# Optimization experiments

Measured on AMD Instinct MI355X. Metric: run time of the kernel, lower is better.

Reference implementation:

```python
import jax, jax.numpy as jnp
import numpy as np

EMB = 128
SQRT_EMB = 128 ** 0.5
LOGIT_CLIP = 10.0


def setup_inputs() -> dict:
    key = jax.random.key(0)
    ks = jax.random.split(key, 10)
    B, N, M, D = 128, 512, 512, EMB
    s = 1.0 / np.sqrt(D)
    return {
        "encoded_last_node": jax.random.normal(ks[0], (B, N, D), jnp.float32),
        "load": jax.random.uniform(ks[1], (B, N), jnp.float32),
        "cur_dist": jax.random.uniform(ks[2], (B, N, M), jnp.float32),
        "log_scale": jnp.ones((), jnp.float32),
        "ninf_mask": jnp.zeros((B, N, M), jnp.float32),
        "encoded_nodes": jax.random.normal(ks[3], (B, M, D), jnp.float32),
        "Wq_last": jax.random.normal(ks[4], (D, D + 1), jnp.float32) * s,
        "Wk": jax.random.normal(ks[5], (D, D), jnp.float32) * s,
        "Wv": jax.random.normal(ks[6], (D, D), jnp.float32) * s,
        "alpha1": jnp.ones((1,), jnp.float32),
        "alpha2": jnp.ones((1,), jnp.float32),
    }


def reference(encoded_last_node, load, cur_dist, log_scale, ninf_mask,
              encoded_nodes, Wq_last, Wk, Wv, alpha1, alpha2):
    # set_kv
    k = jnp.einsum('bmd,ed->bme', encoded_nodes, Wk)   # (B,M,D)
    v = jnp.einsum('bmd,ed->bme', encoded_nodes, Wv)   # (B,M,D)
    # query from last node + load
    input_cat = jnp.concatenate([encoded_last_node, load[:, :, None]], axis=2)  # (B,N,D+1)
    q = jnp.einsum('bnc,ec->bne', input_cat, Wq_last)  # (B,N,D)
    # AAFM: exp-bias linear attention with sigmoid gate
    adaptation_bias = -alpha1[0] * log_scale * cur_dist + ninf_mask  # (B,N,M)
    eb = jnp.exp(adaptation_bias)
    ek = jnp.exp(k)
    num = jnp.einsum('bnm,bmd->bnd', eb, ek * v)
    den = jnp.einsum('bnm,bmd->bnd', eb, ek)
    weighted = jnp.nan_to_num(num / den)  # mirrors torch nan_to_num correction
    aafm_out = jax.nn.sigmoid(q) * weighted  # (B,N,D)
    # single-head decode score against encoder embeddings
    score = jnp.einsum('bnd,bmd->bnm', aafm_out, encoded_nodes)
    score_scaled = score / SQRT_EMB - alpha2[0] * log_scale * cur_dist
    score_masked = LOGIT_CLIP * jnp.tanh(score_scaled) + ninf_mask
    probs = jax.nn.softmax(score_masked, axis=-1)
    return probs
```

## Files before the change

kernel.cpp:

```cpp
#include <hip/hip_runtime.h>
#include <math.h>

#define B 128
#define N 512
#define M 512
#define D 128

typedef __attribute__((ext_vector_type(8))) short s16x8;
typedef __attribute__((ext_vector_type(4))) short s16x4;
typedef __attribute__((ext_vector_type(4))) float f32x4;

#define MFMA16(a, b, c) __builtin_amdgcn_mfma_f32_16x16x32_bf16(a, b, c, 0, 0, 0)

__device__ __forceinline__ void gload16(const void* g, void* l) {
    __builtin_amdgcn_global_load_lds(
        (const __attribute__((address_space(1))) unsigned int*)g,
        (__attribute__((address_space(3))) unsigned int*)l, 16, 0, 0);
}

__device__ __forceinline__ float fast_tanh(float x) {
    x = fminf(fmaxf(x, -15.f), 15.f);
    float E = __expf(2.f * x);
    return 1.f - 2.f / (E + 1.f);
}

__device__ __forceinline__ void fsplit(float x, short& h, short& l) {
    unsigned u = __float_as_uint(x);
    h = (short)(u >> 16);
    float fh = __uint_as_float(u & 0xffff0000u);
    l = (short)(__float_as_uint(x - fh) >> 16);
}

__device__ __forceinline__ void fsplit8(float4 x0, float4 x1, s16x8& h, s16x8& l) {
    short a, b;
    fsplit(x0.x, a, b); h[0] = a; l[0] = b;
    fsplit(x0.y, a, b); h[1] = a; l[1] = b;
    fsplit(x0.z, a, b); h[2] = a; l[2] = b;
    fsplit(x0.w, a, b); h[3] = a; l[3] = b;
    fsplit(x1.x, a, b); h[4] = a; l[4] = b;
    fsplit(x1.y, a, b); h[5] = a; l[5] = b;
    fsplit(x1.z, a, b); h[6] = a; l[6] = b;
    fsplit(x1.w, a, b); h[7] = a; l[7] = b;
}

__global__ void k_prep_w(const float* __restrict__ Wk, const float* __restrict__ Wv,
                         const float* __restrict__ Wq,
                         unsigned short* __restrict__ Wk_hi, unsigned short* __restrict__ Wk_lo,
                         unsigned short* __restrict__ Wv_hi, unsigned short* __restrict__ Wv_lo,
                         unsigned short* __restrict__ Wq_hi, unsigned short* __restrict__ Wq_lo) {
    int i = blockIdx.x * 256 + threadIdx.x;
    short h, l;
    if (i < 16384) {
        fsplit(Wk[i], h, l); Wk_hi[i] = (unsigned short)h; Wk_lo[i] = (unsigned short)l;
    } else if (i < 32768) {
        int j = i - 16384;
        fsplit(Wv[j], h, l); Wv_hi[j] = (unsigned short)h; Wv_lo[j] = (unsigned short)l;
    } else {
        int j = i - 32768; int e = j >> 7, d = j & 127;
        fsplit(Wq[e * 129 + d], h, l); Wq_hi[j] = (unsigned short)h; Wq_lo[j] = (unsigned short)l;
    }
}

__global__ __launch_bounds__(256) void k_kv(const float* __restrict__ enc,
        const unsigned short* __restrict__ Wk_hi, const unsigned short* __restrict__ Wk_lo,
        const unsigned short* __restrict__ Wv_hi, const unsigned short* __restrict__ Wv_lo,
        unsigned short* __restrict__ EKT_hi, unsigned short* __restrict__ EKT_lo,
        unsigned short* __restrict__ EKVT_hi, unsigned short* __restrict__ EKVT_lo) {
    int b = blockIdx.y;
    int wave = threadIdx.x >> 6, lane = threadIdx.x & 63;
    int row = lane & 15, kg = lane >> 4;
    int m0 = blockIdx.x * 64 + wave * 16;
    f32x4 acc[16];
#pragma unroll
    for (int i = 0; i < 16; i++) acc[i] = (f32x4)0.f;
    const float* ap = enc + ((size_t)b * M + m0 + row) * D + kg * 8;
#pragma unroll
    for (int ks = 0; ks < 4; ks++) {
        float4 x0 = *(const float4*)(ap + ks * 32);
        float4 x1 = *(const float4*)(ap + ks * 32 + 4);
        s16x8 ah, al;
        fsplit8(x0, x1, ah, al);
        int wb = ks * 32 + kg * 8;
#pragma unroll
        for (int ct = 0; ct < 8; ct++) {
            int e = ct * 16 + row;
            s16x8 bh = *(const s16x8*)(Wk_hi + e * D + wb);
            s16x8 bl = *(const s16x8*)(Wk_lo + e * D + wb);
            acc[ct] = MFMA16(ah, bh, acc[ct]);
            acc[ct] = MFMA16(al, bh, acc[ct]);
            acc[ct] = MFMA16(ah, bl, acc[ct]);
            bh = *(const s16x8*)(Wv_hi + e * D + wb);
            bl = *(const s16x8*)(Wv_lo + e * D + wb);
            acc[8 + ct] = MFMA16(ah, bh, acc[8 + ct]);
            acc[8 + ct] = MFMA16(al, bh, acc[8 + ct]);
            acc[8 + ct] = MFMA16(ah, bl, acc[8 + ct]);
        }
    }
#pragma unroll
    for (int ct = 0; ct < 8; ct++) {
        int e = ct * 16 + row;
        s16x4 ekh, ekl, evh, evl;
#pragma unroll
        for (int r = 0; r < 4; r++) {
            float ek = __expf(acc[ct][r]);
            float ev = ek * acc[8 + ct][r];
            short h, l;
            fsplit(ek, h, l); ekh[r] = h; ekl[r] = l;
            fsplit(ev, h, l); evh[r] = h; evl[r] = l;
        }
        int m = m0 + kg * 4;
        int chunk = (m & 31) >> 3;
        int p = chunk ^ (e & 3);
        size_t o = ((size_t)b * D + e) * M + (size_t)(m & ~31) + p * 8 + (m & 7);
        *(s16x4*)(EKT_hi + o) = ekh;
        *(s16x4*)(EKT_lo + o) = ekl;
        *(s16x4*)(EKVT_hi + o) = evh;
        *(s16x4*)(EKVT_lo + o) = evl;
    }
}

__global__ __launch_bounds__(256) void k_q(const float* __restrict__ encl,
        const float* __restrict__ loadv, const float* __restrict__ Wq,
        const unsigned short* __restrict__ Wq_hi, const unsigned short* __restrict__ Wq_lo,
        float* __restrict__ SQ) {
    int b = blockIdx.y;
    int wave = threadIdx.x >> 6, lane = threadIdx.x & 63;
    int row = lane & 15, kg = lane >> 4;
    int n0 = blockIdx.x * 64 + wave * 16;
    f32x4 acc[8];
#pragma unroll
    for (int i = 0; i < 8; i++) acc[i] = (f32x4)0.f;
    const float* ap = encl + ((size_t)b * N + n0 + row) * D + kg * 8;
#pragma unroll
    for (int ks = 0; ks < 4; ks++) {
        float4 x0 = *(const float4*)(ap + ks * 32);
        float4 x1 = *(const float4*)(ap + ks * 32 + 4);
        s16x8 ah, al;
        fsplit8(x0, x1, ah, al);
        int wb = ks * 32 + kg * 8;
#pragma unroll
        for (int ct = 0; ct < 8; ct++) {
            int e = ct * 16 + row;
            s16x8 bh = *(const s16x8*)(Wq_hi + e * D + wb);
            s16x8 bl = *(const s16x8*)(Wq_lo + e * D + wb);
            acc[ct] = MFMA16(ah, bh, acc[ct]);
            acc[ct] = MFMA16(al, bh, acc[ct]);
            acc[ct] = MFMA16(ah, bl, acc[ct]);
        }
    }
#pragma unroll
    for (int r = 0; r < 4; r++) {
        int n = n0 + kg * 4 + r;
        float lv = loadv[(size_t)b * N + n];
        size_t ro = ((size_t)b * N + n) * D;
#pragma unroll
        for (int ct = 0; ct < 8; ct++) {
            int e = ct * 16 + row;
            float q = acc[ct][r] + lv * Wq[e * 129 + 128];
            SQ[ro + e] = 1.f / (1.f + __expf(-q));
        }
    }
}

__global__ __launch_bounds__(256) void k_numden(
        const float* __restrict__ cd, const float* __restrict__ ninf,
        const unsigned short* __restrict__ EKVT_hi, const unsigned short* __restrict__ EKVT_lo,
        const unsigned short* __restrict__ EKT_hi, const unsigned short* __restrict__ EKT_lo,
        float* __restrict__ SQ,
        const float* __restrict__ a1p, const float* __restrict__ lsp) {
    int o = blockIdx.x;
    int jj = o >> 3;
    int b = (o & 7) + ((jj >> 3) << 3);
    int nb = jj & 7;
    int w = threadIdx.x >> 6, lane = threadIdx.x & 63;
    int row = lane & 15, kg = lane >> 4;
    int n0 = nb * 64 + w * 16;
    __shared__ __align__(16) char lds[2][32768];
    float a1ls = a1p[0] * lsp[0];
    const char* gbase = (const char*)(w == 0 ? EKVT_hi : w == 1 ? EKVT_lo
                                    : w == 2 ? EKT_hi : EKT_lo)
                        + (size_t)b * D * M * 2;
    int srow = lane >> 2, schunk = lane & 3;
    f32x4 acc[16];
#pragma unroll
    for (int i = 0; i < 16; i++) acc[i] = (f32x4)0.f;
    const float* cdp = cd + ((size_t)b * N + n0 + row) * M + kg * 8;
    const float* nfp = ninf + ((size_t)b * N + n0 + row) * M + kg * 8;
    int rb = row * 64 + ((kg ^ (row & 3)) << 4);

#define STAGE_ND(buf, mt)                                                          \
    _Pragma("unroll")                                                              \
    for (int jv = 0; jv < 8; jv++) {                                               \
        gload16(gbase + (size_t)(jv * 16 + srow) * 1024 + (mt) * 64 + schunk * 16, \
                lds[buf] + w * 8192 + jv * 1024 + lane * 16);                      \
    }

    float4 c0 = *(const float4*)(cdp), c1 = *(const float4*)(cdp + 4);
    float4 f0 = *(const float4*)(nfp), f1 = *(const float4*)(nfp + 4);
    STAGE_ND(0, 0)

#pragma unroll
    for (int mt = 0; mt < 16; mt++) {
        int cur = mt & 1;
        __syncthreads();
        float4 e0, e1;
        e0.x = __expf(fmaf(-a1ls, c0.x, f0.x));
        e0.y = __expf(fmaf(-a1ls, c0.y, f0.y));
        e0.z = __expf(fmaf(-a1ls, c0.z, f0.z));
        e0.w = __expf(fmaf(-a1ls, c0.w, f0.w));
        e1.x = __expf(fmaf(-a1ls, c1.x, f1.x));
        e1.y = __expf(fmaf(-a1ls, c1.y, f1.y));
        e1.z = __expf(fmaf(-a1ls, c1.z, f1.z));
        e1.w = __expf(fmaf(-a1ls, c1.w, f1.w));
        s16x8 ah, al;
        fsplit8(e0, e1, ah, al);
        if (mt < 15) {
            int m = (mt + 1) * 32;
            c0 = *(const float4*)(cdp + m); c1 = *(const float4*)(cdp + m + 4);
            f0 = *(const float4*)(nfp + m); f1 = *(const float4*)(nfp + m + 4);
            STAGE_ND(cur ^ 1, mt + 1)
        }
#pragma unroll
        for (int ct = 0; ct < 8; ct++) {
            int ro = ct * 1024 + rb;
            s16x8 bh = *(const s16x8*)(&lds[cur][ro]);
            s16x8 bl = *(const s16x8*)(&lds[cur][8192 + ro]);
            acc[ct] = MFMA16(ah, bh, acc[ct]);
            acc[ct] = MFMA16(al, bh, acc[ct]);
            acc[ct] = MFMA16(ah, bl, acc[ct]);
            bh = *(const s16x8*)(&lds[cur][16384 + ro]);
            bl = *(const s16x8*)(&lds[cur][24576 + ro]);
            acc[8 + ct] = MFMA16(ah, bh, acc[8 + ct]);
            acc[8 + ct] = MFMA16(al, bh, acc[8 + ct]);
            acc[8 + ct] = MFMA16(ah, bl, acc[8 + ct]);
        }
    }
#pragma unroll
    for (int r = 0; r < 4; r++) {
        int n = n0 + kg * 4 + r;
        size_t ro = ((size_t)b * N + n) * D;
#pragma unroll
        for (int ct = 0; ct < 8; ct++) {
            int e = ct * 16 + row;
            float num = acc[ct][r], den = acc[8 + ct][r];
            float ww = (den != 0.f) ? num / den : 0.f;
            float aafm = SQ[ro + e] * ww;
            unsigned u = __float_as_uint(aafm);
            unsigned hi = u >> 16;
            float fh = __uint_as_float(u & 0xffff0000u);
            unsigned lo = __float_as_uint(aafm - fh) >> 16;
            SQ[ro + e] = __uint_as_float(hi | (lo << 16));
        }
    }
}

__global__ void k_encsplit(const float* __restrict__ enc,
                           unsigned short* __restrict__ Eh, unsigned short* __restrict__ El) {
    size_t i = (size_t)blockIdx.x * 256 + threadIdx.x;
    size_t bm = i >> 4;
    int c = (int)(i & 15);
    int m = (int)(bm & 511);
    int p = c ^ (m & 7);
    const float* src = enc + bm * 128 + c * 8;
    float4 x0 = *(const float4*)(src);
    float4 x1 = *(const float4*)(src + 4);
    s16x8 h, l;
    fsplit8(x0, x1, h, l);
    *(s16x8*)(Eh + bm * 128 + p * 8) = h;
    *(s16x8*)(El + bm * 128 + p * 8) = l;
}

__global__ __launch_bounds__(256) void k_score(
        const float* __restrict__ AAFM,
        const unsigned short* __restrict__ Eh, const unsigned short* __restrict__ El,
        const float* __restrict__ cd, const float* __restrict__ ninf,
        const float* __restrict__ a2p, const float* __restrict__ lsp,
        float* __restrict__ out) {
    int o = blockIdx.x;
    int j = o >> 3;
    int b = (o & 7) + ((j >> 4) << 3);
    int nb = j & 15;
    int n0 = nb * 32;
    int w = threadIdx.x >> 6, lane = threadIdx.x & 63;
    int row = lane & 15, kg = lane >> 4;
    int ng = w >> 1, mh = w & 1;
    __shared__ __align__(16) char lds[2][32768];
    __shared__ float redm[64][2];
    __shared__ float reds[64][2];
    float a2ls = a2p[0] * lsp[0];
    const float invs = 0.08838834764831845f;

    const float* apk = AAFM + ((size_t)b * N + n0 + ng * 16 + row) * D + kg * 8;
    s16x8 ah[4], al[4];
#pragma unroll
    for (int es = 0; es < 4; es++) {
        float4 w0 = *(const float4*)(apk + es * 32);
        float4 w1 = *(const float4*)(apk + es * 32 + 4);
        unsigned u;
        u = __float_as_uint(w0.x); ah[es][0] = (short)(u & 0xffff); al[es][0] = (short)(u >> 16);
        u = __float_as_uint(w0.y); ah[es][1] = (short)(u & 0xffff); al[es][1] = (short)(u >> 16);
        u = __float_as_uint(w0.z); ah[es][2] = (short)(u & 0xffff); al[es][2] = (short)(u >> 16);
        u = __float_as_uint(w0.w); ah[es][3] = (short)(u & 0xffff); al[es][3] = (short)(u >> 16);
        u = __float_as_uint(w1.x); ah[es][4] = (short)(u & 0xffff); al[es][4] = (short)(u >> 16);
        u = __float_as_uint(w1.y); ah[es][5] = (short)(u & 0xffff); al[es][5] = (short)(u >> 16);
        u = __float_as_uint(w1.z); ah[es][6] = (short)(u & 0xffff); al[es][6] = (short)(u >> 16);
        u = __float_as_uint(w1.w); ah[es][7] = (short)(u & 0xffff); al[es][7] = (short)(u >> 16);
    }
    f32x4 acc[16];
#pragma unroll
    for (int i = 0; i < 16; i++) acc[i] = (f32x4)0.f;

#define STAGE_SC(buf, mc)                                                              \
    _Pragma("unroll")                                                                  \
    for (int jv = 0; jv < 8; jv++) {                                                   \
        int flat = w * 8 + jv;                                                         \
        int arr = flat >> 4, wi = flat & 15;                                           \
        const unsigned short* gb = arr ? El : Eh;                                      \
        const char* src = (const char*)gb                                             \
            + ((size_t)b * M + (mc) * 64 + wi * 4 + kg) * 256 + row * 16;              \
        gload16(src, lds[buf] + arr * 16384 + wi * 1024 + lane * 16);                  \
    }

    STAGE_SC(0, 0)
#pragma unroll
    for (int mc = 0; mc < 8; mc++) {
        int cur = mc & 1;
        __syncthreads();
#pragma unroll
        for (int ct = 0; ct < 2; ct++) {
            int mloc = mh * 32 + ct * 16 + row;
            int a = mc * 2 + ct;
            int rbase = mloc * 256;
            int sw = mloc & 7;
#pragma unroll
            for (int es = 0; es < 4; es++) {
                int ph = (4 * es + kg) ^ sw;
                s16x8 bh = *(const s16x8*)(&lds[cur][rbase + ph * 16]);
                s16x8 bl = *(const s16x8*)(&lds[cur][16384 + rbase + ph * 16]);
                acc[a] = MFMA16(ah[es], bh, acc[a]);
                acc[a] = MFMA16(al[es], bh, acc[a]);
                acc[a] = MFMA16(ah[es], bl, acc[a]);
            }
        }
        float cdv[2][4], nfv[2][4];
#pragma unroll
        for (int ct = 0; ct < 2; ct++)
#pragma unroll
            for (int r = 0; r < 4; r++) {
                size_t idx = ((size_t)b * N + n0 + ng * 16 + kg * 4 + r) * M
                           + (size_t)mc * 64 + mh * 32 + ct * 16 + row;
                cdv[ct][r] = cd[idx];
                nfv[ct][r] = ninf[idx];
            }
        if (mc < 7) STAGE_SC(cur ^ 1, mc + 1)
#pragma unroll
        for (int ct = 0; ct < 2; ct++) {
            int a = mc * 2 + ct;
#pragma unroll
            for (int r = 0; r < 4; r++) {
                acc[a][r] = 10.f * fast_tanh(fmaf(acc[a][r], invs, -a2ls * cdv[ct][r]))
                          + nfv[ct][r];
            }
        }
    }
    float mx[4], sm[4];
#pragma unroll
    for (int r = 0; r < 4; r++) {
        float m = acc[0][r];
#pragma unroll
        for (int a = 1; a < 16; a++) m = fmaxf(m, acc[a][r]);
#pragma unroll
        for (int s = 1; s < 16; s <<= 1) m = fmaxf(m, __shfl_xor(m, s, 64));
        mx[r] = m;
    }
    int rl = ng * 16 + kg * 4;
    if (row == 0) {
#pragma unroll
        for (int r = 0; r < 4; r++) redm[rl + r][mh] = mx[r];
    }
    __syncthreads();
#pragma unroll
    for (int r = 0; r < 4; r++) {
        float m = fmaxf(redm[rl + r][0], redm[rl + r][1]);
        float s = 0.f;
#pragma unroll
        for (int a = 0; a < 16; a++) {
            float e = __expf(acc[a][r] - m);
            acc[a][r] = e;
            s += e;
        }
#pragma unroll
        for (int sh = 1; sh < 16; sh <<= 1) s += __shfl_xor(s, sh, 64);
        sm[r] = s;
    }
    if (row == 0) {
#pragma unroll
        for (int r = 0; r < 4; r++) reds[rl + r][mh] = sm[r];
    }
    __syncthreads();
    float inv[4];
#pragma unroll
    for (int r = 0; r < 4; r++)
        inv[r] = 1.f / (reds[rl + r][0] + reds[rl + r][1]);
#pragma unroll
    for (int a = 0; a < 16; a++) {
        int mc = a >> 1, ct = a & 1;
        size_t mb = (size_t)mc * 64 + mh * 32 + ct * 16 + row;
#pragma unroll
        for (int r = 0; r < 4; r++) {
            int n = n0 + ng * 16 + kg * 4 + r;
            out[((size_t)b * N + n) * M + mb] = acc[a][r] * inv[r];
        }
    }
}

extern "C" void kernel_launch(void* const* d_in, const int* in_sizes, int n_in,
                              void* d_out, int out_size, void* d_ws, size_t ws_size,
                              hipStream_t stream) {
    const float* encl  = (const float*)d_in[0];
    const float* loadv = (const float*)d_in[1];
    const float* cdist = (const float*)d_in[2];
    const float* ls    = (const float*)d_in[3];
    const float* ninf  = (const float*)d_in[4];
    const float* enc   = (const float*)d_in[5];
    const float* Wq    = (const float*)d_in[6];
    const float* Wk    = (const float*)d_in[7];
    const float* Wv    = (const float*)d_in[8];
    const float* a1    = (const float*)d_in[9];
    const float* a2    = (const float*)d_in[10];
    char* ws = (char*)d_ws;
    unsigned short* EKT_hi  = (unsigned short*)(ws);
    unsigned short* EKT_lo  = (unsigned short*)(ws + 16777216);
    unsigned short* EKVT_hi = (unsigned short*)(ws + 33554432);
    unsigned short* EKVT_lo = (unsigned short*)(ws + 50331648);
    float*          SQ      = (float*)(ws + 67108864);
    unsigned short* Wk_hi   = (unsigned short*)(ws + 100663296);
    unsigned short* Wk_lo   = (unsigned short*)(ws + 100663296 + 32768);
    unsigned short* Wv_hi   = (unsigned short*)(ws + 100663296 + 65536);
    unsigned short* Wv_lo   = (unsigned short*)(ws + 100663296 + 98304);
    unsigned short* Wq_hi   = (unsigned short*)(ws + 100663296 + 131072);
    unsigned short* Wq_lo   = (unsigned short*)(ws + 100663296 + 163840);
    unsigned short* ENC_hi  = EKT_hi;
    unsigned short* ENC_lo  = EKT_lo;
    float* out = (float*)d_out;

    k_prep_w<<<192, 256, 0, stream>>>(Wk, Wv, Wq, Wk_hi, Wk_lo, Wv_hi, Wv_lo, Wq_hi, Wq_lo);
    k_kv<<<dim3(8, 128), 256, 0, stream>>>(enc, Wk_hi, Wk_lo, Wv_hi, Wv_lo,
                                           EKT_hi, EKT_lo, EKVT_hi, EKVT_lo);
    k_q<<<dim3(8, 128), 256, 0, stream>>>(encl, loadv, Wq, Wq_hi, Wq_lo, SQ);
    k_numden<<<1024, 256, 0, stream>>>(cdist, ninf, EKVT_hi, EKVT_lo,
                                       EKT_hi, EKT_lo, SQ, a1, ls);
    k_encsplit<<<4096, 256, 0, stream>>>(enc, ENC_hi, ENC_lo);
    k_score<<<2048, 256, 0, stream>>>(SQ, ENC_hi, ENC_lo, cdist, ninf, a2, ls, out);
}
```

Measured before the change: 376.7 us.

## Double rows per wave in numden and score kernels to reuse staged B tiles

```diff
diff --git a/kernel.cpp b/kernel.cpp
--- a/kernel.cpp
+++ b/kernel.cpp
@@ -41,6 +41,20 @@
     fsplit(x1.y, a, b); h[5] = a; l[5] = b;
     fsplit(x1.z, a, b); h[6] = a; l[6] = b;
     fsplit(x1.w, a, b); h[7] = a; l[7] = b;
+}
+
+__device__ __forceinline__ void ebsplit(float4 c0, float4 c1, float4 f0, float4 f1,
+                                        float a1ls, s16x8& ah, s16x8& al) {
+    float4 e0, e1;
+    e0.x = __expf(fmaf(-a1ls, c0.x, f0.x));
+    e0.y = __expf(fmaf(-a1ls, c0.y, f0.y));
+    e0.z = __expf(fmaf(-a1ls, c0.z, f0.z));
+    e0.w = __expf(fmaf(-a1ls, c0.w, f0.w));
+    e1.x = __expf(fmaf(-a1ls, c1.x, f1.x));
+    e1.y = __expf(fmaf(-a1ls, c1.y, f1.y));
+    e1.z = __expf(fmaf(-a1ls, c1.z, f1.z));
+    e1.w = __expf(fmaf(-a1ls, c1.w, f1.w));
+    fsplit8(e0, e1, ah, al);
 }
 
 __global__ void k_prep_w(const float* __restrict__ Wk, const float* __restrict__ Wv,
@@ -162,30 +176,34 @@
     }
 }
 
-__global__ __launch_bounds__(256) void k_numden(
+__global__ __launch_bounds__(256, 2) void k_numden(
         const float* __restrict__ cd, const float* __restrict__ ninf,
         const unsigned short* __restrict__ EKVT_hi, const unsigned short* __restrict__ EKVT_lo,
         const unsigned short* __restrict__ EKT_hi, const unsigned short* __restrict__ EKT_lo,
         float* __restrict__ SQ,
         const float* __restrict__ a1p, const float* __restrict__ lsp) {
     int o = blockIdx.x;
-    int jj = o >> 3;
-    int b = (o & 7) + ((jj >> 3) << 3);
-    int nb = jj & 7;
+    int xcd = o & 7, j = o >> 3;
+    int b = ((j >> 2) << 3) + xcd;
+    int nb = j & 3;
     int w = threadIdx.x >> 6, lane = threadIdx.x & 63;
     int row = lane & 15, kg = lane >> 4;
-    int n0 = nb * 64 + w * 16;
+    int n0 = nb * 128 + w * 32;
     __shared__ __align__(16) char lds[2][32768];
     float a1ls = a1p[0] * lsp[0];
     const char* gbase = (const char*)(w == 0 ? EKVT_hi : w == 1 ? EKVT_lo
                                     : w == 2 ? EKT_hi : EKT_lo)
                         + (size_t)b * D * M * 2;
     int srow = lane >> 2, schunk = lane & 3;
-    f32x4 acc[16];
-#pragma unroll
-    for (int i = 0; i < 16; i++) acc[i] = (f32x4)0.f;
-    const float* cdp = cd + ((size_t)b * N + n0 + row) * M + kg * 8;
-    const float* nfp = ninf + ((size_t)b * N + n0 + row) * M + kg * 8;
+    f32x4 accN[2][8], accD[2][8];
+#pragma unroll
+    for (int s = 0; s < 2; s++)
+#pragma unroll
+        for (int i = 0; i < 8; i++) { accN[s][i] = (f32x4)0.f; accD[s][i] = (f32x4)0.f; }
+    const float* cdp0 = cd + ((size_t)b * N + n0 + row) * M + kg * 8;
+    const float* nfp0 = ninf + ((size_t)b * N + n0 + row) * M + kg * 8;
+    const float* cdp1 = cdp0 + (size_t)16 * M;
+    const float* nfp1 = nfp0 + (size_t)16 * M;
     int rb = row * 64 + ((kg ^ (row & 3)) << 4);
 
 #define STAGE_ND(buf, mt)                                                          \
@@ -195,29 +213,25 @@
                 lds[buf] + w * 8192 + jv * 1024 + lane * 16);                      \
     }
 
-    float4 c0 = *(const float4*)(cdp), c1 = *(const float4*)(cdp + 4);
-    float4 f0 = *(const float4*)(nfp), f1 = *(const float4*)(nfp + 4);
+    float4 c00 = *(const float4*)(cdp0), c01 = *(const float4*)(cdp0 + 4);
+    float4 f00 = *(const float4*)(nfp0), f01 = *(const float4*)(nfp0 + 4);
+    float4 c10 = *(const float4*)(cdp1), c11 = *(const float4*)(cdp1 + 4);
+    float4 f10 = *(const float4*)(nfp1), f11 = *(const float4*)(nfp1 + 4);
     STAGE_ND(0, 0)
 
-#pragma unroll
+#pragma unroll 2
     for (int mt = 0; mt < 16; mt++) {
         int cur = mt & 1;
         __syncthreads();
-        float4 e0, e1;
-        e0.x = __expf(fmaf(-a1ls, c0.x, f0.x));
-        e0.y = __expf(fmaf(-a1ls, c0.y, f0.y));
-        e0.z = __expf(fmaf(-a1ls, c0.z, f0.z));
-        e0.w = __expf(fmaf(-a1ls, c0.w, f0.w));
-        e1.x = __expf(fmaf(-a1ls, c1.x, f1.x));
-        e1.y = __expf(fmaf(-a1ls, c1.y, f1.y));
-        e1.z = __expf(fmaf(-a1ls, c1.z, f1.z));
-        e1.w = __expf(fmaf(-a1ls, c1.w, f1.w));
-        s16x8 ah, al;
-        fsplit8(e0, e1, ah, al);
+        s16x8 ah0, al0, ah1, al1;
+        ebsplit(c00, c01, f00, f01, a1ls, ah0, al0);
+        ebsplit(c10, c11, f10, f11, a1ls, ah1, al1);
         if (mt < 15) {
             int m = (mt + 1) * 32;
-            c0 = *(const float4*)(cdp + m); c1 = *(const float4*)(cdp + m + 4);
-            f0 = *(const float4*)(nfp + m); f1 = *(const float4*)(nfp + m + 4);
+            c00 = *(const float4*)(cdp0 + m); c01 = *(const float4*)(cdp0 + m + 4);
+            f00 = *(const float4*)(nfp0 + m); f01 = *(const float4*)(nfp0 + m + 4);
+            c10 = *(const float4*)(cdp1 + m); c11 = *(const float4*)(cdp1 + m + 4);
+            f10 = *(const float4*)(nfp1 + m); f11 = *(const float4*)(nfp1 + m + 4);
             STAGE_ND(cur ^ 1, mt + 1)
         }
 #pragma unroll
@@ -225,31 +239,40 @@
             int ro = ct * 1024 + rb;
             s16x8 bh = *(const s16x8*)(&lds[cur][ro]);
             s16x8 bl = *(const s16x8*)(&lds[cur][8192 + ro]);
-            acc[ct] = MFMA16(ah, bh, acc[ct]);
-            acc[ct] = MFMA16(al, bh, acc[ct]);
-            acc[ct] = MFMA16(ah, bl, acc[ct]);
+            accN[0][ct] = MFMA16(ah0, bh, accN[0][ct]);
+            accN[0][ct] = MFMA16(al0, bh, accN[0][ct]);
+            accN[0][ct] = MFMA16(ah0, bl, accN[0][ct]);
+            accN[1][ct] = MFMA16(ah1, bh, accN[1][ct]);
+            accN[1][ct] = MFMA16(al1, bh, accN[1][ct]);
+            accN[1][ct] = MFMA16(ah1, bl, accN[1][ct]);
             bh = *(const s16x8*)(&lds[cur][16384 + ro]);
             bl = *(const s16x8*)(&lds[cur][24576 + ro]);
-            acc[8 + ct] = MFMA16(ah, bh, acc[8 + ct]);
-            acc[8 + ct] = MFMA16(al, bh, acc[8 + ct]);
-            acc[8 + ct] = MFMA16(ah, bl, acc[8 + ct]);
-        }
-    }
-#pragma unroll
-    for (int r = 0; r < 4; r++) {
-        int n = n0 + kg * 4 + r;
-        size_t ro = ((size_t)b * N + n) * D;
-#pragma unroll
-        for (int ct = 0; ct < 8; ct++) {
-            int e = ct * 16 + row;
-            float num = acc[ct][r], den = acc[8 + ct][r];
-            float ww = (den != 0.f) ? num / den : 0.f;
-            float aafm = SQ[ro + e] * ww;
-            unsigned u = __float_as_uint(aafm);
-            unsigned hi = u >> 16;
-            float fh = __uint_as_float(u & 0xffff0000u);
-            unsigned lo = __float_as_uint(aafm - fh) >> 16;
-            SQ[ro + e] = __uint_as_float(hi | (lo << 16));
+            accD[0][ct] = MFMA16(ah0, bh, accD[0][ct]);
+            accD[0][ct] = MFMA16(al0, bh, accD[0][ct]);
+            accD[0][ct] = MFMA16(ah0, bl, accD[0][ct]);
+            accD[1][ct] = MFMA16(ah1, bh, accD[1][ct]);
+            accD[1][ct] = MFMA16(al1, bh, accD[1][ct]);
+            accD[1][ct] = MFMA16(ah1, bl, accD[1][ct]);
+        }
+    }
+#pragma unroll
+    for (int s = 0; s < 2; s++) {
+#pragma unroll
+        for (int r = 0; r < 4; r++) {
+            int n = n0 + s * 16 + kg * 4 + r;
+            size_t ro = ((size_t)b * N + n) * D;
+#pragma unroll
+            for (int ct = 0; ct < 8; ct++) {
+                int e = ct * 16 + row;
+                float num = accN[s][ct][r], den = accD[s][ct][r];
+                float ww = (den != 0.f) ? num / den : 0.f;
+                float aafm = SQ[ro + e] * ww;
+                unsigned u = __float_as_uint(aafm);
+                unsigned hi = u >> 16;
+                float fh = __uint_as_float(u & 0xffff0000u);
+                unsigned lo = __float_as_uint(aafm - fh) >> 16;
+                SQ[ro + e] = __uint_as_float(hi | (lo << 16));
+            }
         }
     }
 }
@@ -270,17 +293,17 @@
     *(s16x8*)(El + bm * 128 + p * 8) = l;
 }
 
-__global__ __launch_bounds__(256) void k_score(
+__global__ __launch_bounds__(256, 2) void k_score(
         const float* __restrict__ AAFM,
         const unsigned short* __restrict__ Eh, const unsigned short* __restrict__ El,
         const float* __restrict__ cd, const float* __restrict__ ninf,
         const float* __restrict__ a2p, const float* __restrict__ lsp,
         float* __restrict__ out) {
     int o = blockIdx.x;
-    int j = o >> 3;
-    int b = (o & 7) + ((j >> 4) << 3);
-    int nb = j & 15;
-    int n0 = nb * 32;
+    int xcd = o & 7, j = o >> 3;
+    int b = ((j >> 3) << 3) + xcd;
+    int nb = j & 7;
+    int n0 = nb * 64;
     int w = threadIdx.x >> 6, lane = threadIdx.x & 63;
     int row = lane & 15, kg = lane >> 4;
     int ng = w >> 1, mh = w & 1;
@@ -290,25 +313,30 @@
     float a2ls = a2p[0] * lsp[0];
     const float invs = 0.08838834764831845f;
 
-    const float* apk = AAFM + ((size_t)b * N + n0 + ng * 16 + row) * D + kg * 8;
-    s16x8 ah[4], al[4];
-#pragma unroll
-    for (int es = 0; es < 4; es++) {
-        float4 w0 = *(const float4*)(apk + es * 32);
-        float4 w1 = *(const float4*)(apk + es * 32 + 4);
-        unsigned u;
-        u = __float_as_uint(w0.x); ah[es][0] = (short)(u & 0xffff); al[es][0] = (short)(u >> 16);
-        u = __float_as_uint(w0.y); ah[es][1] = (short)(u & 0xffff); al[es][1] = (short)(u >> 16);
-        u = __float_as_uint(w0.z); ah[es][2] = (short)(u & 0xffff); al[es][2] = (short)(u >> 16);
-        u = __float_as_uint(w0.w); ah[es][3] = (short)(u & 0xffff); al[es][3] = (short)(u >> 16);
-        u = __float_as_uint(w1.x); ah[es][4] = (short)(u & 0xffff); al[es][4] = (short)(u >> 16);
-        u = __float_as_uint(w1.y); ah[es][5] = (short)(u & 0xffff); al[es][5] = (short)(u >> 16);
-        u = __float_as_uint(w1.z); ah[es][6] = (short)(u & 0xffff); al[es][6] = (short)(u >> 16);
-        u = __float_as_uint(w1.w); ah[es][7] = (short)(u & 0xffff); al[es][7] = (short)(u >> 16);
-    }
-    f32x4 acc[16];
-#pragma unroll
-    for (int i = 0; i < 16; i++) acc[i] = (f32x4)0.f;
+    s16x8 ah[2][4], al[2][4];
+#pragma unroll
+    for (int s = 0; s < 2; s++) {
+        const float* apk = AAFM + ((size_t)b * N + n0 + ng * 32 + s * 16 + row) * D + kg * 8;
+#pragma unroll
+        for (int es = 0; es < 4; es++) {
+            float4 w0 = *(const float4*)(apk + es * 32);
+            float4 w1 = *(const float4*)(apk + es * 32 + 4);
+            unsigned u;
+            u = __float_as_uint(w0.x); ah[s][es][0] = (short)(u & 0xffff); al[s][es][0] = (short)(u >> 16);
+            u = __float_as_uint(w0.y); ah[s][es][1] = (short)(u & 0xffff); al[s][es][1] = (short)(u >> 16);
+            u = __float_as_uint(w0.z); ah[s][es][2] = (short)(u & 0xffff); al[s][es][2] = (short)(u >> 16);
+            u = __float_as_uint(w0.w); ah[s][es][3] = (short)(u & 0xffff); al[s][es][3] = (short)(u >> 16);
+            u = __float_as_uint(w1.x); ah[s][es][4] = (short)(u & 0xffff); al[s][es][4] = (short)(u >> 16);
+            u = __float_as_uint(w1.y); ah[s][es][5] = (short)(u & 0xffff); al[s][es][5] = (short)(u >> 16);
+            u = __float_as_uint(w1.z); ah[s][es][6] = (short)(u & 0xffff); al[s][es][6] = (short)(u >> 16);
+            u = __float_as_uint(w1.w); ah[s][es][7] = (short)(u & 0xffff); al[s][es][7] = (short)(u >> 16);
+        }
+    }
+    f32x4 acc[2][16];
+#pragma unroll
+    for (int s = 0; s < 2; s++)
+#pragma unroll
+        for (int i = 0; i < 16; i++) acc[s][i] = (f32x4)0.f;
 
 #define STAGE_SC(buf, mc)                                                              \
     _Pragma("unroll")                                                                  \
@@ -337,79 +365,95 @@
                 int ph = (4 * es + kg) ^ sw;
                 s16x8 bh = *(const s16x8*)(&lds[cur][rbase + ph * 16]);
                 s16x8 bl = *(const s16x8*)(&lds[cur][16384 + rbase + ph * 16]);
-                acc[a] = MFMA16(ah[es], bh, acc[a]);
-                acc[a] = MFMA16(al[es], bh, acc[a]);
-                acc[a] = MFMA16(ah[es], bl, acc[a]);
+                acc[0][a] = MFMA16(ah[0][es], bh, acc[0][a]);
+                acc[0][a] = MFMA16(al[0][es], bh, acc[0][a]);
+                acc[0][a] = MFMA16(ah[0][es], bl, acc[0][a]);
+                acc[1][a] = MFMA16(ah[1][es], bh, acc[1][a]);
+                acc[1][a] = MFMA16(al[1][es], bh, acc[1][a]);
+                acc[1][a] = MFMA16(ah[1][es], bl, acc[1][a]);
             }
         }
-        float cdv[2][4], nfv[2][4];
-#pragma unroll
-        for (int ct = 0; ct < 2; ct++)
-#pragma unroll
-            for (int r = 0; r < 4; r++) {
-                size_t idx = ((size_t)b * N + n0 + ng * 16 + kg * 4 + r) * M
-                           + (size_t)mc * 64 + mh * 32 + ct * 16 + row;
-                cdv[ct][r] = cd[idx];
-                nfv[ct][r] = ninf[idx];
+        float cdv[2][2][4], nfv[2][2][4];
+#pragma unroll
+        for (int s = 0; s < 2; s++)
+#pragma unroll
+            for (int ct = 0; ct < 2; ct++)
+#pragma unroll
+                for (int r = 0; r < 4; r++) {
+                    size_t idx = ((size_t)b * N + n0 + ng * 32 + s * 16 + kg * 4 + r) * M
+                               + (size_t)mc * 64 + mh * 32 + ct * 16 + row;
+                    cdv[s][ct][r] = cd[idx];
+                    nfv[s][ct][r] = ninf[idx];
+                }
+        if (mc < 7) STAGE_SC(cur ^ 1, mc + 1)
+#pragma unroll
+        for (int s = 0; s < 2; s++)
+#pragma unroll
+            for (int ct = 0; ct < 2; ct++) {
+                int a = mc * 2 + ct;
+#pragma unroll
+                for (int r = 0; r < 4; r++) {
+                    acc[s][a][r] = 10.f * fast_tanh(fmaf(acc[s][a][r], invs,
+                                                         -a2ls * cdv[s][ct][r]))
+                                 + nfv[s][ct][r];
+                }
             }
-        if (mc < 7) STAGE_SC(cur ^ 1, mc + 1)
-#pragma unroll
-        for (int ct = 0; ct < 2; ct++) {
-            int a = mc * 2 + ct;
-#pragma unroll
-            for (int r = 0; r < 4; r++) {
-                acc[a][r] = 10.f * fast_tanh(fmaf(acc[a][r], invs, -a2ls * cdv[ct][r]))
-                          + nfv[ct][r];
+    }
+    float mx[2][4], sm[2][4];
+#pragma unroll
+    for (int s = 0; s < 2; s++)
+#pragma unroll
+        for (int r = 0; r < 4; r++) {
+            float m = acc[s][0][r];
+#pragma unroll
+            for (int a = 1; a < 16; a++) m = fmaxf(m, acc[s][a][r]);
+#pragma unroll
+            for (int sh = 1; sh < 16; sh <<= 1) m = fmaxf(m, __shfl_xor(m, sh, 64));
+            mx[s][r] = m;
+        }
+    if (row == 0) {
+#pragma unroll
+        for (int s = 0; s < 2; s++)
+#pragma unroll
+            for (int r = 0; r < 4; r++) redm[ng * 32 + s * 16 + kg * 4 + r][mh] = mx[s][r];
+    }
+    __syncthreads();
+#pragma unroll
+    for (int s = 0; s < 2; s++)
+#pragma unroll
+        for (int r = 0; r < 4; r++) {
+            int rl = ng * 32 + s * 16 + kg * 4 + r;
+            float m = fmaxf(redm[rl][0], redm[rl][1]);
+            float sum = 0.f;
+#pragma unroll
+            for (int a = 0; a < 16; a++) {
+                float e = __expf(acc[s][a][r] - m);
+                acc[s][a][r] = e;
+                sum += e;
             }
-        }
-    }
-    float mx[4], sm[4];
-#pragma unroll
-    for (int r = 0; r < 4; r++) {
-        float m = acc[0][r];
-#pragma unroll
-        for (int a = 1; a < 16; a++) m = fmaxf(m, acc[a][r]);
-#pragma unroll
-        for (int s = 1; s < 16; s <<= 1) m = fmaxf(m, __shfl_xor(m, s, 64));
-        mx[r] = m;
-    }
-    int rl = ng * 16 + kg * 4;
+#pragma unroll
+            for (int sh = 1; sh < 16; sh <<= 1) sum += __shfl_xor(sum, sh, 64);
+            sm[s][r] = sum;
+        }
     if (row == 0) {
 #pragma unroll
-        for (int r = 0; r < 4; r++) redm[rl + r][mh] = mx[r];
+        for (int s = 0; s < 2; s++)
+#pragma unroll
+            for (int r = 0; r < 4; r++) reds[ng * 32 + s * 16 + kg * 4 + r][mh] = sm[s][r];
     }
     __syncthreads();
 #pragma unroll
-    for (int r = 0; r < 4; r++) {
-        float m = fmaxf(redm[rl + r][0], redm[rl + r][1]);
-        float s = 0.f;
-#pragma unroll
-        for (int a = 0; a < 16; a++) {
-            float e = __expf(acc[a][r] - m);
-            acc[a][r] = e;
-            s += e;
-        }
-#pragma unroll
-        for (int sh = 1; sh < 16; sh <<= 1) s += __shfl_xor(s, sh, 64);
-        sm[r] = s;
-    }
-    if (row == 0) {
-#pragma unroll
-        for (int r = 0; r < 4; r++) reds[rl + r][mh] = sm[r];
-    }
-    __syncthreads();
-    float inv[4];
-#pragma unroll
-    for (int r = 0; r < 4; r++)
-        inv[r] = 1.f / (reds[rl + r][0] + reds[rl + r][1]);
-#pragma unroll
-    for (int a = 0; a < 16; a++) {
-        int mc = a >> 1, ct = a & 1;
-        size_t mb = (size_t)mc * 64 + mh * 32 + ct * 16 + row;
+    for (int s = 0; s < 2; s++) {
 #pragma unroll
         for (int r = 0; r < 4; r++) {
-            int n = n0 + ng * 16 + kg * 4 + r;
-            out[((size_t)b * N + n) * M + mb] = acc[a][r] * inv[r];
+            int rl = ng * 32 + s * 16 + kg * 4 + r;
+            float inv = 1.f / (reds[rl][0] + reds[rl][1]);
+            size_t ro = ((size_t)b * N + n0 + rl) * M;
+#pragma unroll
+            for (int a = 0; a < 16; a++) {
+                size_t mb = (size_t)(a >> 1) * 64 + mh * 32 + (a & 1) * 16 + row;
+                out[ro + mb] = acc[s][a][r] * inv;
+            }
         }
     }
 }
@@ -448,8 +492,8 @@
     k_kv<<<dim3(8, 128), 256, 0, stream>>>(enc, Wk_hi, Wk_lo, Wv_hi, Wv_lo,
                                            EKT_hi, EKT_lo, EKVT_hi, EKVT_lo);
     k_q<<<dim3(8, 128), 256, 0, stream>>>(encl, loadv, Wq, Wq_hi, Wq_lo, SQ);
-    k_numden<<<1024, 256, 0, stream>>>(cdist, ninf, EKVT_hi, EKVT_lo,
-                                       EKT_hi, EKT_lo, SQ, a1, ls);
+    k_numden<<<512, 256, 0, stream>>>(cdist, ninf, EKVT_hi, EKVT_lo,
+                                      EKT_hi, EKT_lo, SQ, a1, ls);
     k_encsplit<<<4096, 256, 0, stream>>>(enc, ENC_hi, ENC_lo);
-    k_score<<<2048, 256, 0, stream>>>(SQ, ENC_hi, ENC_lo, cdist, ninf, a2, ls, out);
-}
+    k_score<<<1024, 256, 0, stream>>>(SQ, ENC_hi, ENC_lo, cdist, ninf, a2, ls, out);
+}
```

Measured after the change: 363.5 us. 3.5% less time.

## Switch numden to 32x32 MFMA tiles and halve LDS stages for occupancy

Applied to the files above, without the earlier changes.

```diff
diff --git a/kernel.cpp b/kernel.cpp
--- a/kernel.cpp
+++ b/kernel.cpp
@@ -9,8 +9,10 @@
 typedef __attribute__((ext_vector_type(8))) short s16x8;
 typedef __attribute__((ext_vector_type(4))) short s16x4;
 typedef __attribute__((ext_vector_type(4))) float f32x4;
+typedef __attribute__((ext_vector_type(16))) float f32x16;
 
 #define MFMA16(a, b, c) __builtin_amdgcn_mfma_f32_16x16x32_bf16(a, b, c, 0, 0, 0)
+#define MFMA32(a, b, c) __builtin_amdgcn_mfma_f32_32x32x16_bf16(a, b, c, 0, 0, 0)
 
 __device__ __forceinline__ void gload16(const void* g, void* l) {
     __builtin_amdgcn_global_load_lds(
@@ -41,6 +43,20 @@
     fsplit(x1.y, a, b); h[5] = a; l[5] = b;
     fsplit(x1.z, a, b); h[6] = a; l[6] = b;
     fsplit(x1.w, a, b); h[7] = a; l[7] = b;
+}
+
+__device__ __forceinline__ void ebsplit(float4 c0, float4 c1, float4 f0, float4 f1,
+                                        float a1ls, s16x8& ah, s16x8& al) {
+    float4 e0, e1;
+    e0.x = __expf(fmaf(-a1ls, c0.x, f0.x));
+    e0.y = __expf(fmaf(-a1ls, c0.y, f0.y));
+    e0.z = __expf(fmaf(-a1ls, c0.z, f0.z));
+    e0.w = __expf(fmaf(-a1ls, c0.w, f0.w));
+    e1.x = __expf(fmaf(-a1ls, c1.x, f1.x));
+    e1.y = __expf(fmaf(-a1ls, c1.y, f1.y));
+    e1.z = __expf(fmaf(-a1ls, c1.z, f1.z));
+    e1.w = __expf(fmaf(-a1ls, c1.w, f1.w));
+    fsplit8(e0, e1, ah, al);
 }
 
 __global__ void k_prep_w(const float* __restrict__ Wk, const float* __restrict__ Wv,
@@ -108,10 +124,8 @@
             fsplit(ek, h, l); ekh[r] = h; ekl[r] = l;
             fsplit(ev, h, l); evh[r] = h; evl[r] = l;
         }
-        int m = m0 + kg * 4;
-        int chunk = (m & 31) >> 3;
-        int p = chunk ^ (e & 3);
-        size_t o = ((size_t)b * D + e) * M + (size_t)(m & ~31) + p * 8 + (m & 7);
+        int p = (kg >> 1) ^ (e & 1);
+        size_t o = ((size_t)b * D + e) * M + m0 + p * 8 + (kg & 1) * 4;
         *(s16x4*)(EKT_hi + o) = ekh;
         *(s16x4*)(EKT_lo + o) = ekl;
         *(s16x4*)(EKVT_hi + o) = evh;
@@ -162,94 +176,100 @@
     }
 }
 
-__global__ __launch_bounds__(256) void k_numden(
+__global__ __launch_bounds__(256, 3) void k_numden(
         const float* __restrict__ cd, const float* __restrict__ ninf,
         const unsigned short* __restrict__ EKVT_hi, const unsigned short* __restrict__ EKVT_lo,
         const unsigned short* __restrict__ EKT_hi, const unsigned short* __restrict__ EKT_lo,
         float* __restrict__ SQ,
         const float* __restrict__ a1p, const float* __restrict__ lsp) {
     int o = blockIdx.x;
-    int jj = o >> 3;
-    int b = (o & 7) + ((jj >> 3) << 3);
-    int nb = jj & 7;
+    int xcd = o & 7, j = o >> 3;
+    int b = ((j >> 3) << 3) + xcd;
+    int nb = j & 7;
     int w = threadIdx.x >> 6, lane = threadIdx.x & 63;
-    int row = lane & 15, kg = lane >> 4;
-    int n0 = nb * 64 + w * 16;
-    __shared__ __align__(16) char lds[2][32768];
+    int ng = w >> 1, eh = w & 1;
+    int col = lane & 31, kh = lane >> 5;
+    int n0 = nb * 64 + ng * 32;
+    __shared__ __align__(16) char lds[2][16384];
     float a1ls = a1p[0] * lsp[0];
     const char* gbase = (const char*)(w == 0 ? EKVT_hi : w == 1 ? EKVT_lo
                                     : w == 2 ? EKT_hi : EKT_lo)
                         + (size_t)b * D * M * 2;
-    int srow = lane >> 2, schunk = lane & 3;
-    f32x4 acc[16];
-#pragma unroll
-    for (int i = 0; i < 16; i++) acc[i] = (f32x4)0.f;
-    const float* cdp = cd + ((size_t)b * N + n0 + row) * M + kg * 8;
-    const float* nfp = ninf + ((size_t)b * N + n0 + row) * M + kg * 8;
-    int rb = row * 64 + ((kg ^ (row & 3)) << 4);
-
-#define STAGE_ND(buf, mt)                                                          \
-    _Pragma("unroll")                                                              \
-    for (int jv = 0; jv < 8; jv++) {                                               \
-        gload16(gbase + (size_t)(jv * 16 + srow) * 1024 + (mt) * 64 + schunk * 16, \
-                lds[buf] + w * 8192 + jv * 1024 + lane * 16);                      \
+    f32x16 accN0 = (f32x16)0.f, accN1 = (f32x16)0.f;
+    f32x16 accD0 = (f32x16)0.f, accD1 = (f32x16)0.f;
+    const float* cdp = cd + ((size_t)b * N + n0 + col) * M + kh * 8;
+    const float* nfp = ninf + ((size_t)b * N + n0 + col) * M + kh * 8;
+    int rb = eh * 2048 + col * 32 + ((kh ^ (lane & 1)) << 4);
+
+#define STAGE_ND(buf, mt)                                                      \
+    _Pragma("unroll")                                                          \
+    for (int jv = 0; jv < 4; jv++) {                                           \
+        int flat = jv * 64 + lane;                                             \
+        gload16(gbase + (size_t)(flat >> 1) * 1024 + (mt) * 32 + (flat & 1) * 16, \
+                lds[buf] + w * 4096 + flat * 16);                              \
     }
 
     float4 c0 = *(const float4*)(cdp), c1 = *(const float4*)(cdp + 4);
     float4 f0 = *(const float4*)(nfp), f1 = *(const float4*)(nfp + 4);
     STAGE_ND(0, 0)
 
-#pragma unroll
-    for (int mt = 0; mt < 16; mt++) {
+#pragma unroll 2
+    for (int mt = 0; mt < 32; mt++) {
         int cur = mt & 1;
         __syncthreads();
-        float4 e0, e1;
-        e0.x = __expf(fmaf(-a1ls, c0.x, f0.x));
-        e0.y = __expf(fmaf(-a1ls, c0.y, f0.y));
-        e0.z = __expf(fmaf(-a1ls, c0.z, f0.z));
-        e0.w = __expf(fmaf(-a1ls, c0.w, f0.w));
-        e1.x = __expf(fmaf(-a1ls, c1.x, f1.x));
-        e1.y = __expf(fmaf(-a1ls, c1.y, f1.y));
-        e1.z = __expf(fmaf(-a1ls, c1.z, f1.z));
-        e1.w = __expf(fmaf(-a1ls, c1.w, f1.w));
         s16x8 ah, al;
-        fsplit8(e0, e1, ah, al);
-        if (mt < 15) {
-            int m = (mt + 1) * 32;
+        ebsplit(c0, c1, f0, f1, a1ls, ah, al);
+        if (mt < 31) {
+            int m = (mt + 1) * 16;
             c0 = *(const float4*)(cdp + m); c1 = *(const float4*)(cdp + m + 4);
             f0 = *(const float4*)(nfp + m); f1 = *(const float4*)(nfp + m + 4);
             STAGE_ND(cur ^ 1, mt + 1)
         }
-#pragma unroll
-        for (int ct = 0; ct < 8; ct++) {
-            int ro = ct * 1024 + rb;
-            s16x8 bh = *(const s16x8*)(&lds[cur][ro]);
-            s16x8 bl = *(const s16x8*)(&lds[cur][8192 + ro]);
-            acc[ct] = MFMA16(ah, bh, acc[ct]);
-            acc[ct] = MFMA16(al, bh, acc[ct]);
-            acc[ct] = MFMA16(ah, bl, acc[ct]);
-            bh = *(const s16x8*)(&lds[cur][16384 + ro]);
-            bl = *(const s16x8*)(&lds[cur][24576 + ro]);
-            acc[8 + ct] = MFMA16(ah, bh, acc[8 + ct]);
-            acc[8 + ct] = MFMA16(al, bh, acc[8 + ct]);
-            acc[8 + ct] = MFMA16(ah, bl, acc[8 + ct]);
-        }
-    }
-#pragma unroll
-    for (int r = 0; r < 4; r++) {
-        int n = n0 + kg * 4 + r;
-        size_t ro = ((size_t)b * N + n) * D;
-#pragma unroll
-        for (int ct = 0; ct < 8; ct++) {
-            int e = ct * 16 + row;
-            float num = acc[ct][r], den = acc[8 + ct][r];
+        const char* L = lds[cur];
+        {
+            int roff = rb;
+            s16x8 vh = *(const s16x8*)(L + roff);
+            s16x8 vl = *(const s16x8*)(L + 4096 + roff);
+            s16x8 th = *(const s16x8*)(L + 8192 + roff);
+            s16x8 tl = *(const s16x8*)(L + 12288 + roff);
+            accN0 = MFMA32(ah, vh, accN0);
+            accN0 = MFMA32(al, vh, accN0);
+            accN0 = MFMA32(ah, vl, accN0);
+            accD0 = MFMA32(ah, th, accD0);
+            accD0 = MFMA32(al, th, accD0);
+            accD0 = MFMA32(ah, tl, accD0);
+        }
+        {
+            int roff = 1024 + rb;
+            s16x8 vh = *(const s16x8*)(L + roff);
+            s16x8 vl = *(const s16x8*)(L + 4096 + roff);
+            s16x8 th = *(const s16x8*)(L + 8192 + roff);
+            s16x8 tl = *(const s16x8*)(L + 12288 + roff);
+            accN1 = MFMA32(ah, vh, accN1);
+            accN1 = MFMA32(al, vh, accN1);
+            accN1 = MFMA32(ah, vl, accN1);
+            accD1 = MFMA32(ah, th, accD1);
+            accD1 = MFMA32(al, th, accD1);
+            accD1 = MFMA32(ah, tl, accD1);
+        }
+    }
+    size_t rowbase = ((size_t)b * N + n0 + 4 * kh) * D + eh * 64 + col;
+#pragma unroll
+    for (int et = 0; et < 2; et++) {
+        f32x16 aN = et ? accN1 : accN0;
+        f32x16 aD = et ? accD1 : accD0;
+#pragma unroll
+        for (int r = 0; r < 16; r++) {
+            int dn = (r & 3) + 8 * (r >> 2);
+            size_t idx = rowbase + (size_t)dn * D + et * 32;
+            float num = aN[r], den = aD[r];
             float ww = (den != 0.f) ? num / den : 0.f;
-            float aafm = SQ[ro + e] * ww;
+            float aafm = SQ[idx] * ww;
             unsigned u = __float_as_uint(aafm);
             unsigned hi = u >> 16;
             float fh = __uint_as_float(u & 0xffff0000u);
             unsigned lo = __float_as_uint(aafm - fh) >> 16;
-            SQ[ro + e] = __uint_as_float(hi | (lo << 16));
+            SQ[idx] = __uint_as_float(hi | (lo << 16));
         }
     }
 }
@@ -270,23 +290,23 @@
     *(s16x8*)(El + bm * 128 + p * 8) = l;
 }
 
-__global__ __launch_bounds__(256) void k_score(
+__global__ __launch_bounds__(256, 3) void k_score(
         const float* __restrict__ AAFM,
         const unsigned short* __restrict__ Eh, const unsigned short* __restrict__ El,
         const float* __restrict__ cd, const float* __restrict__ ninf,
         const float* __restrict__ a2p, const float* __restrict__ lsp,
         float* __restrict__ out) {
     int o = blockIdx.x;
-    int j = o >> 3;
-    int b = (o & 7) + ((j >> 4) << 3);
+    int xcd = o & 7, j = o >> 3;
+    int b = ((j >> 4) << 3) + xcd;
     int nb = j & 15;
     int n0 = nb * 32;
     int w = threadIdx.x >> 6, lane = threadIdx.x & 63;
     int row = lane & 15, kg = lane >> 4;
     int ng = w >> 1, mh = w & 1;
-    __shared__ __align__(16) char lds[2][32768];
-    __shared__ float redm[64][2];
-    __shared__ float reds[64][2];
+    __shared__ __align__(16) char lds[2][16384];
+    __shared__ float redm[32][2];
+    __shared__ float reds[32][2];
     float a2ls = a2p[0] * lsp[0];
     const float invs = 0.08838834764831845f;
 
@@ -310,57 +330,46 @@
 #pragma unroll
     for (int i = 0; i < 16; i++) acc[i] = (f32x4)0.f;
 
-#define STAGE_SC(buf, mc)                                                              \
-    _Pragma("unroll")                                                                  \
-    for (int jv = 0; jv < 8; jv++) {                                                   \
-        int flat = w * 8 + jv;                                                         \
-        int arr = flat >> 4, wi = flat & 15;                                           \
-        const unsigned short* gb = arr ? El : Eh;                                      \
-        const char* src = (const char*)gb                                             \
-            + ((size_t)b * M + (mc) * 64 + wi * 4 + kg) * 256 + row * 16;              \
-        gload16(src, lds[buf] + arr * 16384 + wi * 1024 + lane * 16);                  \
+#define STAGE_SC(buf, mc)                                                          \
+    _Pragma("unroll")                                                              \
+    for (int jv = 0; jv < 4; jv++) {                                               \
+        int id = (w * 4 + jv) * 64 + lane;                                         \
+        int arr = id >> 9, rem = id & 511;                                         \
+        const unsigned short* gb = arr ? El : Eh;                                  \
+        gload16((const char*)gb + ((size_t)b * M + (mc) * 32) * 256 + rem * 16,    \
+                lds[buf] + arr * 8192 + rem * 16);                                 \
     }
 
     STAGE_SC(0, 0)
 #pragma unroll
-    for (int mc = 0; mc < 8; mc++) {
+    for (int mc = 0; mc < 16; mc++) {
         int cur = mc & 1;
         __syncthreads();
-#pragma unroll
-        for (int ct = 0; ct < 2; ct++) {
-            int mloc = mh * 32 + ct * 16 + row;
-            int a = mc * 2 + ct;
-            int rbase = mloc * 256;
-            int sw = mloc & 7;
-#pragma unroll
-            for (int es = 0; es < 4; es++) {
-                int ph = (4 * es + kg) ^ sw;
-                s16x8 bh = *(const s16x8*)(&lds[cur][rbase + ph * 16]);
-                s16x8 bl = *(const s16x8*)(&lds[cur][16384 + rbase + ph * 16]);
-                acc[a] = MFMA16(ah[es], bh, acc[a]);
-                acc[a] = MFMA16(al[es], bh, acc[a]);
-                acc[a] = MFMA16(ah[es], bl, acc[a]);
-            }
-        }
-        float cdv[2][4], nfv[2][4];
-#pragma unroll
-        for (int ct = 0; ct < 2; ct++)
-#pragma unroll
-            for (int r = 0; r < 4; r++) {
-                size_t idx = ((size_t)b * N + n0 + ng * 16 + kg * 4 + r) * M
-                           + (size_t)mc * 64 + mh * 32 + ct * 16 + row;
-                cdv[ct][r] = cd[idx];
-                nfv[ct][r] = ninf[idx];
-            }
-        if (mc < 7) STAGE_SC(cur ^ 1, mc + 1)
-#pragma unroll
-        for (int ct = 0; ct < 2; ct++) {
-            int a = mc * 2 + ct;
-#pragma unroll
-            for (int r = 0; r < 4; r++) {
-                acc[a][r] = 10.f * fast_tanh(fmaf(acc[a][r], invs, -a2ls * cdv[ct][r]))
-                          + nfv[ct][r];
-            }
+        int mloc = mh * 16 + row;
+        int rbase = mloc * 256;
+        int sw = mloc & 7;
+#pragma unroll
+        for (int es = 0; es < 4; es++) {
+            int ph = (4 * es + kg) ^ sw;
+            s16x8 bh = *(const s16x8*)(&lds[cur][rbase + ph * 16]);
+            s16x8 bl = *(const s16x8*)(&lds[cur][8192 + rbase + ph * 16]);
+            acc[mc] = MFMA16(ah[es], bh, acc[mc]);
+            acc[mc] = MFMA16(al[es], bh, acc[mc]);
+            acc[mc] = MFMA16(ah[es], bl, acc[mc]);
+        }
+        float cdv[4], nfv[4];
+#pragma unroll
+        for (int r = 0; r < 4; r++) {
+            size_t idx = ((size_t)b * N + n0 + ng * 16 + kg * 4 + r) * M
+                       + (size_t)mc * 32 + mloc;
+            cdv[r] = cd[idx];
+            nfv[r] = ninf[idx];
+        }
+        if (mc < 15) STAGE_SC(cur ^ 1, mc + 1)
+#pragma unroll
+        for (int r = 0; r < 4; r++) {
+            acc[mc][r] = 10.f * fast_tanh(fmaf(acc[mc][r], invs, -a2ls * cdv[r]))
+                       + nfv[r];
         }
     }
     float mx[4], sm[4];
@@ -398,18 +407,13 @@
         for (int r = 0; r < 4; r++) reds[rl + r][mh] = sm[r];
     }
     __syncthreads();
-    float inv[4];
-#pragma unroll
-    for (int r = 0; r < 4; r++)
-        inv[r] = 1.f / (reds[rl + r][0] + reds[rl + r][1]);
-#pragma unroll
-    for (int a = 0; a < 16; a++) {
-        int mc = a >> 1, ct = a & 1;
-        size_t mb = (size_t)mc * 64 + mh * 32 + ct * 16 + row;
-#pragma unroll
-        for (int r = 0; r < 4; r++) {
-            int n = n0 + ng * 16 + kg * 4 + r;
-            out[((size_t)b * N + n) * M + mb] = acc[a][r] * inv[r];
+#pragma unroll
+    for (int r = 0; r < 4; r++) {
+        float inv = 1.f / (reds[rl + r][0] + reds[rl + r][1]);
+        size_t ro = ((size_t)b * N + n0 + rl + r) * M;
+#pragma unroll
+        for (int a = 0; a < 16; a++) {
+            out[ro + a * 32 + mh * 16 + row] = acc[a][r] * inv;
         }
     }
 }
```

Measured after the change: 432.6 us. 1.15x slower.
